# Kernel optimization log

Measured on AMD Instinct MI355X. Metric: run time of the kernel, lower is better.

Reference implementation:

```python
import jax, jax.numpy as jnp
import numpy as np


def setup_inputs() -> dict:
    key = jax.random.key(0)
    k1, k2, k3 = jax.random.split(key, 3)
    B, S, Q, K, D = 64, 512, 800, 4, 64
    q_data = jax.random.normal(k1, (B, S, Q), dtype=jnp.float32)
    r_data = jax.random.randint(k2, (B, S), 0, K)
    # learned params (xavier-ish scale)
    Wq = jax.random.normal(k3, (D, Q), dtype=jnp.float32) * (0.5 * (2.0 / (Q + D)) ** 0.5)
    bq = jnp.zeros((D,), dtype=jnp.float32)
    Wr = jax.random.normal(jax.random.fold_in(key, 7), (1, K), dtype=jnp.float32) * (0.5 * (2.0 / (K + 1)) ** 0.5)
    br = jnp.zeros((1,), dtype=jnp.float32)
    return {"q_data": q_data, "r_data": r_data, "Wq": Wq, "bq": bq,
            "Wr": Wr, "br": br, "n_questions": Q, "n_cats": K}


def reference(q_data, r_data, Wq, bq, Wr, br, n_questions, n_cats):
    # Vectorized over (batch, seq): original looped over t in python.
    K = n_cats
    k_idx = jnp.arange(K, dtype=q_data.dtype)                      # [K]
    dist = jnp.abs(k_idx[None, None, :] - r_data[..., None].astype(q_data.dtype)) / (K - 1)  # [B,S,K]
    weights = jnp.maximum(1.0 - dist, 0.0)                        # [B,S,K]
    # response_weights: Linear(K -> 1) then sigmoid -> scalar gate per (b,s)
    gate = jax.nn.sigmoid(jnp.einsum('bsk,ok->bso', weights, Wr) + br)  # [B,S,1]
    weighted_q = q_data * gate                                    # [B,S,Q]
    # question_embed: Linear(Q -> D)
    out = jnp.einsum('bsq,dq->bsd', weighted_q, Wq) + bq          # [B,S,D]
    return out
```

## Files before the change

kernel.cpp:

```cpp
#include <hip/hip_runtime.h>
#include <hip/hip_bf16.h>


#define QD 800
#define DD 64
#define M_TOTAL 32768
#define KT 25

typedef __attribute__((ext_vector_type(8))) short bf16x8;
typedef __attribute__((ext_vector_type(4))) float f32x4;

static __device__ __forceinline__ short f2bf(float f) {
  union { __hip_bfloat16 h; short s; } u;
  u.h = __float2bfloat16(f);
  return u.s;
}

static __device__ __forceinline__ bf16x8 load_split8(const float* __restrict__ p) {
  f32x4 lo = *reinterpret_cast<const f32x4*>(p);
  f32x4 hi = *reinterpret_cast<const f32x4*>(p + 16);
  bf16x8 r;
  r[0] = f2bf(lo.x); r[1] = f2bf(lo.y); r[2] = f2bf(lo.z); r[3] = f2bf(lo.w);
  r[4] = f2bf(hi.x); r[5] = f2bf(hi.y); r[6] = f2bf(hi.z); r[7] = f2bf(hi.w);
  return r;
}

__global__ __launch_bounds__(256, 2) void sold_kernel(
    const float* __restrict__ q, const int* __restrict__ rdat,
    const float* __restrict__ Wq, const float* __restrict__ bq,
    const float* __restrict__ Wr, const float* __restrict__ br,
    float* __restrict__ out) {
  const int lane = threadIdx.x & 63;
  const int wave = threadIdx.x >> 6;
  const int l15 = lane & 15;
  const int lhi = lane >> 4;
  const int m0 = blockIdx.x * 64 + wave * 16;

  const float* aptr = q + (size_t)(m0 + l15) * QD + lhi * 4;
  const float* w0 = Wq + (0 * 16 + l15) * QD + lhi * 4;
  const float* w1 = Wq + (1 * 16 + l15) * QD + lhi * 4;
  const float* w2 = Wq + (2 * 16 + l15) * QD + lhi * 4;
  const float* w3 = Wq + (3 * 16 + l15) * QD + lhi * 4;

  f32x4 acc0 = {0.f, 0.f, 0.f, 0.f};
  f32x4 acc1 = {0.f, 0.f, 0.f, 0.f};
  f32x4 acc2 = {0.f, 0.f, 0.f, 0.f};
  f32x4 acc3 = {0.f, 0.f, 0.f, 0.f};

#pragma unroll 5
  for (int kt = 0; kt < KT; ++kt) {
    bf16x8 a  = load_split8(aptr + kt * 32);
    bf16x8 b0 = load_split8(w0 + kt * 32);
    bf16x8 b1 = load_split8(w1 + kt * 32);
    bf16x8 b2 = load_split8(w2 + kt * 32);
    bf16x8 b3 = load_split8(w3 + kt * 32);
    acc0 = __builtin_amdgcn_mfma_f32_16x16x32_bf16(a, b0, acc0, 0, 0, 0);
    acc1 = __builtin_amdgcn_mfma_f32_16x16x32_bf16(a, b1, acc1, 0, 0, 0);
    acc2 = __builtin_amdgcn_mfma_f32_16x16x32_bf16(a, b2, acc2, 0, 0, 0);
    acc3 = __builtin_amdgcn_mfma_f32_16x16x32_bf16(a, b3, acc3, 0, 0, 0);
  }

  float wr[4] = {Wr[0], Wr[1], Wr[2], Wr[3]};
  float brv = br[0];
  float lut[4];
  const float inv3 = 1.0f / 3.0f;
#pragma unroll
  for (int r = 0; r < 4; ++r) {
    float s = brv;
#pragma unroll
    for (int k = 0; k < 4; ++k) {
      float w = fmaxf(1.0f - fabsf((float)(k - r)) * inv3, 0.0f);
      s += w * wr[k];
    }
    lut[r] = 1.0f / (1.0f + __expf(-s));
  }

  float bqv0 = bq[0 * 16 + l15];
  float bqv1 = bq[1 * 16 + l15];
  float bqv2 = bq[2 * 16 + l15];
  float bqv3 = bq[3 * 16 + l15];

#pragma unroll
  for (int r = 0; r < 4; ++r) {
    int row = m0 + lhi * 4 + r;
    float g = lut[rdat[row]];
    float* orow = out + (size_t)row * DD + l15;
    orow[0]  = acc0[r] * g + bqv0;
    orow[16] = acc1[r] * g + bqv1;
    orow[32] = acc2[r] * g + bqv2;
    orow[48] = acc3[r] * g + bqv3;
  }
}

extern "C" void kernel_launch(void* const* d_in, const int* in_sizes, int n_in,
                              void* d_out, int out_size, void* d_ws, size_t ws_size,
                              hipStream_t stream) {
  const float* q    = (const float*)d_in[0];
  const int*   rdat = (const int*)d_in[1];
  const float* Wq   = (const float*)d_in[2];
  const float* bq   = (const float*)d_in[3];
  const float* Wr   = (const float*)d_in[4];
  const float* br   = (const float*)d_in[5];
  float* out = (float*)d_out;

  sold_kernel<<<M_TOTAL / 64, 256, 0, stream>>>(q, rdat, Wq, bq, Wr, br, out);
}
```

Baseline: 196.0 us.

## Pre-convert Wq to bf16 fragments and pipeline q loads via global_load_lds

Adds a small pre-pass that converts Wq to bf16 in MFMA fragment order in workspace. The main kernel then streams q tiles and the pre-packed weight tiles into a 3-stage LDS ring using direct global-to-LDS loads, with an XOR swizzle on the q rows. The goal is to hide global load latency and avoid re-converting Wq in every block. It costs an extra kernel launch, a barrier per k-step, and smaller blocks of 128 threads over 32 rows. The old direct kernel remains as a fallback when workspace is too small.

```diff
diff --git a/kernel.cpp b/kernel.cpp
--- a/kernel.cpp
+++ b/kernel.cpp
@@ -1,14 +1,24 @@
 #include <hip/hip_runtime.h>
 #include <hip/hip_bf16.h>
+#include <stdint.h>
 
 
 #define QD 800
 #define DD 64
 #define M_TOTAL 32768
 #define KT 25
+#define PIPE 3
 
 typedef __attribute__((ext_vector_type(8))) short bf16x8;
 typedef __attribute__((ext_vector_type(4))) float f32x4;
+
+typedef const __attribute__((address_space(1))) uint32_t* gas1_u32;
+typedef __attribute__((address_space(3))) uint32_t* las3_u32;
+
+static __device__ __forceinline__ void gll16(const void* g, const void* l) {
+  __builtin_amdgcn_global_load_lds((gas1_u32)(uintptr_t)g,
+                                   (las3_u32)(uint32_t)(uintptr_t)l, 16, 0, 0);
+}
 
 static __device__ __forceinline__ short f2bf(float f) {
   union { __hip_bfloat16 h; short s; } u;
@@ -16,16 +26,131 @@
   return u.s;
 }
 
-static __device__ __forceinline__ bf16x8 load_split8(const float* __restrict__ p) {
-  f32x4 lo = *reinterpret_cast<const f32x4*>(p);
-  f32x4 hi = *reinterpret_cast<const f32x4*>(p + 16);
+static __device__ __forceinline__ bf16x8 pack8(f32x4 lo, f32x4 hi) {
   bf16x8 r;
   r[0] = f2bf(lo.x); r[1] = f2bf(lo.y); r[2] = f2bf(lo.z); r[3] = f2bf(lo.w);
   r[4] = f2bf(hi.x); r[5] = f2bf(hi.y); r[6] = f2bf(hi.z); r[7] = f2bf(hi.w);
   return r;
 }
 
-__global__ __launch_bounds__(256, 2) void sold_kernel(
+static __device__ __forceinline__ bf16x8 load_split8(const float* __restrict__ p) {
+  return pack8(*reinterpret_cast<const f32x4*>(p),
+               *reinterpret_cast<const f32x4*>(p + 16));
+}
+
+__global__ void convert_wq_kernel(const float* __restrict__ Wq, short* __restrict__ Bb) {
+  int idx = blockIdx.x * 256 + threadIdx.x;
+  int kt = idx >> 8;
+  int acc = (idx >> 6) & 3;
+  int lane = idx & 63;
+  int l15 = lane & 15, lhi = lane >> 4;
+  const float* p = Wq + (acc * 16 + l15) * QD + kt * 32 + lhi * 4;
+  *reinterpret_cast<bf16x8*>(Bb + (size_t)idx * 8) = load_split8(p);
+}
+
+static __device__ __forceinline__ void stage(
+    const float* __restrict__ qbase, const short* __restrict__ blob, int kt,
+    float* bufA, short* bufB, int t, int wave) {
+  const float* qk = qbase + kt * 32;
+  const short* bk = blob + (size_t)kt * 2048;
+#pragma unroll
+  for (int j = 0; j < 2; ++j) {
+    int s = j * 128 + t;
+    int row = s >> 3;
+    int kseg = (s & 7) ^ (row & 7);
+    gll16(qk + (size_t)row * QD + kseg * 4, bufA + (j * 128 + wave * 64) * 4);
+  }
+#pragma unroll
+  for (int j = 0; j < 2; ++j) {
+    int s = j * 128 + t;
+    gll16(bk + s * 8, bufB + (j * 128 + wave * 64) * 8);
+  }
+}
+
+__global__ __launch_bounds__(128, 2) void sold_kernel(
+    const float* __restrict__ q, const int* __restrict__ rdat,
+    const short* __restrict__ Bb, const float* __restrict__ bq,
+    const float* __restrict__ Wr, const float* __restrict__ br,
+    float* __restrict__ out) {
+  const int t = threadIdx.x;
+  const int lane = t & 63;
+  const int wave = t >> 6;
+  const int l15 = lane & 15;
+  const int lhi = lane >> 4;
+  const int m0 = blockIdx.x * 32;
+
+  __shared__ __align__(16) float bufA[PIPE][1024];
+  __shared__ __align__(16) short bufB[PIPE][2048];
+
+  const float* qbase = q + (size_t)m0 * QD;
+
+  f32x4 acc0 = {0.f, 0.f, 0.f, 0.f};
+  f32x4 acc1 = {0.f, 0.f, 0.f, 0.f};
+  f32x4 acc2 = {0.f, 0.f, 0.f, 0.f};
+  f32x4 acc3 = {0.f, 0.f, 0.f, 0.f};
+
+  stage(qbase, Bb, 0, bufA[0], bufB[0], t, wave);
+  stage(qbase, Bb, 1, bufA[1], bufB[1], t, wave);
+
+  const int row32 = wave * 16 + l15;
+  const int rb = row32 & 7;
+  const int offA_lo = row32 * 32 + ((0 + lhi) ^ rb) * 4;
+  const int offA_hi = row32 * 32 + ((4 + lhi) ^ rb) * 4;
+
+  for (int kt = 0; kt < KT; ++kt) {
+    __syncthreads();
+    int nx = kt + 2;
+    int sl = kt % PIPE;
+    if (nx < KT) stage(qbase, Bb, nx, bufA[nx % PIPE], bufB[nx % PIPE], t, wave);
+
+    const float* A = bufA[sl];
+    const short* B = bufB[sl];
+    f32x4 alo = *reinterpret_cast<const f32x4*>(A + offA_lo);
+    f32x4 ahi = *reinterpret_cast<const f32x4*>(A + offA_hi);
+    bf16x8 a = pack8(alo, ahi);
+    bf16x8 b0 = *reinterpret_cast<const bf16x8*>(B + (0 * 64 + lane) * 8);
+    bf16x8 b1 = *reinterpret_cast<const bf16x8*>(B + (1 * 64 + lane) * 8);
+    bf16x8 b2 = *reinterpret_cast<const bf16x8*>(B + (2 * 64 + lane) * 8);
+    bf16x8 b3 = *reinterpret_cast<const bf16x8*>(B + (3 * 64 + lane) * 8);
+    acc0 = __builtin_amdgcn_mfma_f32_16x16x32_bf16(a, b0, acc0, 0, 0, 0);
+    acc1 = __builtin_amdgcn_mfma_f32_16x16x32_bf16(a, b1, acc1, 0, 0, 0);
+    acc2 = __builtin_amdgcn_mfma_f32_16x16x32_bf16(a, b2, acc2, 0, 0, 0);
+    acc3 = __builtin_amdgcn_mfma_f32_16x16x32_bf16(a, b3, acc3, 0, 0, 0);
+  }
+
+  float wr[4] = {Wr[0], Wr[1], Wr[2], Wr[3]};
+  float brv = br[0];
+  float lut[4];
+  const float inv3 = 1.0f / 3.0f;
+#pragma unroll
+  for (int r = 0; r < 4; ++r) {
+    float s = brv;
+#pragma unroll
+    for (int k = 0; k < 4; ++k) {
+      float w = fmaxf(1.0f - fabsf((float)(k - r)) * inv3, 0.0f);
+      s += w * wr[k];
+    }
+    lut[r] = 1.0f / (1.0f + __expf(-s));
+  }
+
+  float bqv0 = bq[0 * 16 + l15];
+  float bqv1 = bq[1 * 16 + l15];
+  float bqv2 = bq[2 * 16 + l15];
+  float bqv3 = bq[3 * 16 + l15];
+
+#pragma unroll
+  for (int r = 0; r < 4; ++r) {
+    int row = m0 + wave * 16 + lhi * 4 + r;
+    float g = lut[rdat[row]];
+    float* orow = out + (size_t)row * DD + l15;
+    orow[0]  = acc0[r] * g + bqv0;
+    orow[16] = acc1[r] * g + bqv1;
+    orow[32] = acc2[r] * g + bqv2;
+    orow[48] = acc3[r] * g + bqv3;
+  }
+}
+
+__global__ __launch_bounds__(256, 2) void sold_direct(
     const float* __restrict__ q, const int* __restrict__ rdat,
     const float* __restrict__ Wq, const float* __restrict__ bq,
     const float* __restrict__ Wr, const float* __restrict__ br,
@@ -35,18 +160,13 @@
   const int l15 = lane & 15;
   const int lhi = lane >> 4;
   const int m0 = blockIdx.x * 64 + wave * 16;
-
   const float* aptr = q + (size_t)(m0 + l15) * QD + lhi * 4;
   const float* w0 = Wq + (0 * 16 + l15) * QD + lhi * 4;
   const float* w1 = Wq + (1 * 16 + l15) * QD + lhi * 4;
   const float* w2 = Wq + (2 * 16 + l15) * QD + lhi * 4;
   const float* w3 = Wq + (3 * 16 + l15) * QD + lhi * 4;
-
-  f32x4 acc0 = {0.f, 0.f, 0.f, 0.f};
-  f32x4 acc1 = {0.f, 0.f, 0.f, 0.f};
-  f32x4 acc2 = {0.f, 0.f, 0.f, 0.f};
-  f32x4 acc3 = {0.f, 0.f, 0.f, 0.f};
-
+  f32x4 acc0 = {0.f,0.f,0.f,0.f}, acc1 = {0.f,0.f,0.f,0.f};
+  f32x4 acc2 = {0.f,0.f,0.f,0.f}, acc3 = {0.f,0.f,0.f,0.f};
 #pragma unroll 5
   for (int kt = 0; kt < KT; ++kt) {
     bf16x8 a  = load_split8(aptr + kt * 32);
@@ -59,27 +179,18 @@
     acc2 = __builtin_amdgcn_mfma_f32_16x16x32_bf16(a, b2, acc2, 0, 0, 0);
     acc3 = __builtin_amdgcn_mfma_f32_16x16x32_bf16(a, b3, acc3, 0, 0, 0);
   }
-
   float wr[4] = {Wr[0], Wr[1], Wr[2], Wr[3]};
-  float brv = br[0];
-  float lut[4];
+  float brv = br[0], lut[4];
   const float inv3 = 1.0f / 3.0f;
 #pragma unroll
   for (int r = 0; r < 4; ++r) {
     float s = brv;
 #pragma unroll
-    for (int k = 0; k < 4; ++k) {
-      float w = fmaxf(1.0f - fabsf((float)(k - r)) * inv3, 0.0f);
-      s += w * wr[k];
-    }
+    for (int k = 0; k < 4; ++k)
+      s += fmaxf(1.0f - fabsf((float)(k - r)) * inv3, 0.0f) * wr[k];
     lut[r] = 1.0f / (1.0f + __expf(-s));
   }
-
-  float bqv0 = bq[0 * 16 + l15];
-  float bqv1 = bq[1 * 16 + l15];
-  float bqv2 = bq[2 * 16 + l15];
-  float bqv3 = bq[3 * 16 + l15];
-
+  float bqv0 = bq[l15], bqv1 = bq[16 + l15], bqv2 = bq[32 + l15], bqv3 = bq[48 + l15];
 #pragma unroll
   for (int r = 0; r < 4; ++r) {
     int row = m0 + lhi * 4 + r;
@@ -103,5 +214,12 @@
   const float* br   = (const float*)d_in[5];
   float* out = (float*)d_out;
 
-  sold_kernel<<<M_TOTAL / 64, 256, 0, stream>>>(q, rdat, Wq, bq, Wr, br, out);
-}
+  const size_t need_ws = (size_t)KT * 2048 * sizeof(short);
+  if (ws_size >= need_ws) {
+    short* Bb = (short*)d_ws;
+    convert_wq_kernel<<<KT, 256, 0, stream>>>(Wq, Bb);
+    sold_kernel<<<M_TOTAL / 32, 128, 0, stream>>>(q, rdat, Bb, bq, Wr, br, out);
+  } else {
+    sold_direct<<<M_TOTAL / 64, 256, 0, stream>>>(q, rdat, Wq, bq, Wr, br, out);
+  }
+}
```

Result: faster. 171.3 us (-12.6%).
